# Kernel tuning notes

Measured on AMD Instinct MI355X. Metric: run time of the kernel, lower is better.

## Reference

```python
import jax, jax.numpy as jnp
import numpy as np

NUM_CLASSES = 64
EPSILON = 0.05
BETA1 = 1.0
BETA2 = 1.0
WARM_UP_EPOCH = 10


def _loss(x):
    # log_loss: log(1+exp(-(x-eps))) + log(1+exp(x+eps))
    return jax.nn.softplus(-(x - EPSILON)) + jax.nn.softplus(x + EPSILON)


def _per_class_fac(Y):
    # fac_c = 1 / (N_c * (N_total - N_c)); guarded against degenerate classes
    n = Y.sum(0)
    tot = n.sum()
    ok = (n > 0) & (n < tot)
    return jnp.where(ok, 1.0 / jnp.where(ok, n * (tot - n), 1.0), 0.0)


def _masked_pair_sum(x_cij, Y):
    # x_cij: [C,N,N] pairwise arg; Y: [N,C] one-hot. Sum loss over (pos i, neg j)
    pos = Y.T          # [C,N]
    neg = 1.0 - Y.T    # [C,N]
    return jnp.einsum('cij,ci,cj->c', _loss(x_cij), pos, neg)


def _empirical(preds, Y):
    p = preds.T                              # [C,N]
    d = p[:, :, None] - p[:, None, :]        # [C,N,N] delta_f
    per = _masked_pair_sum(4.0 * (1.0 - d), Y)
    return jnp.sum(_per_class_fac(Y) * per)


def _discrepancy(preds, preds_adv, Y):
    p = preds.T
    pa = preds_adv.T
    d = p[:, :, None] - p[:, None, :]        # delta_f
    da = pa[:, :, None] - pa[:, None, :]     # delta_f_hat
    per = _masked_pair_sum(2.0 * (da - d), Y)
    return jnp.sum(_per_class_fac(Y) * per)


def setup_inputs() -> dict:
    key = jax.random.key(0)
    ks = jax.random.split(key, 5)
    N = 1024
    return {
        'y_s': jax.random.normal(ks[0], (N, NUM_CLASSES), jnp.float32),
        'y_s_adv': jax.random.normal(ks[1], (N, NUM_CLASSES), jnp.float32),
        'labels_s': jax.random.randint(ks[2], (N,), 0, NUM_CLASSES),
        'y_t': jax.random.normal(ks[3], (N, NUM_CLASSES), jnp.float32),
        'y_t_adv': jax.random.normal(ks[4], (N, NUM_CLASSES), jnp.float32),
        'epoch': 10,
    }


def reference(y_s, y_s_adv, labels_s, y_t, y_t_adv, epoch):
    ps = jax.nn.softmax(y_s, axis=-1)
    psa = jax.nn.softmax(y_s_adv, axis=-1)
    Ys = jax.nn.one_hot(labels_s, NUM_CLASSES, dtype=ps.dtype)

    empirical = _empirical(ps, Ys)                      # source empirical AUC error
    src_disc = _discrepancy(ps, psa, Ys)
    transfer = -BETA2 * 0.5 * src_disc

    if epoch >= WARM_UP_EPOCH:  # epoch is a static Python int
        pt = jax.nn.softmax(y_t, axis=-1)
        pta = jax.nn.softmax(y_t_adv, axis=-1)
        # pseudo labels: one-hot of argmax of adversarial-head target probs
        Yt = jax.nn.one_hot(jnp.argmax(pta, axis=-1), NUM_CLASSES, dtype=pt.dtype)
        transfer = transfer + BETA1 * 0.25 * _discrepancy(pt, pta, Yt)

    return (0.25 * empirical, transfer)
```

## Files before the change

kernel.cpp:

```cpp
#include <hip/hip_runtime.h>

#define N 1024
#define C 64
#define CHUNK 256
#define SPLITS (N / CHUNK)

__device__ __forceinline__ float softplus_f(float x) {
    return fmaxf(x, 0.0f) + log1pf(__expf(-fabsf(x)));
}
__device__ __forceinline__ float loss_f(float x) {
    return softplus_f(0.05f - x) + softplus_f(x + 0.05f);
}

__device__ __forceinline__ float softmax64(float x) {
    float m = x;
    #pragma unroll
    for (int off = 32; off; off >>= 1) m = fmaxf(m, __shfl_xor(m, off, 64));
    float e = __expf(x - m);
    float s = e;
    #pragma unroll
    for (int off = 32; off; off >>= 1) s += __shfl_xor(s, off, 64);
    return e / s;
}

__global__ __launch_bounds__(256) void prep_kernel(
    const float* __restrict__ y_s, const float* __restrict__ y_s_adv,
    const float* __restrict__ y_t, const float* __restrict__ y_t_adv,
    float* __restrict__ Ps, float* __restrict__ Qs, float* __restrict__ Qt,
    int* __restrict__ t_labels)
{
    const int lane = threadIdx.x & 63;
    const int row  = blockIdx.x * 4 + (threadIdx.x >> 6);
    if (row >= N) return;
    const int g = row * C + lane;

    float ps  = softmax64(y_s[g]);
    float psa = softmax64(y_s_adv[g]);
    Ps[lane * N + row] = ps;
    Qs[lane * N + row] = psa - ps;

    float xta = y_t_adv[g];
    float pt  = softmax64(y_t[g]);
    float pta = softmax64(xta);
    Qt[lane * N + row] = pta - pt;

    float v = xta; int idx = lane;
    #pragma unroll
    for (int off = 32; off; off >>= 1) {
        float ov = __shfl_xor(v, off, 64);
        int   oi = __shfl_xor(idx, off, 64);
        if (ov > v || (ov == v && oi < idx)) { v = ov; idx = oi; }
    }
    if (lane == 0) t_labels[row] = idx;
}

__global__ __launch_bounds__(256) void pair_kernel(
    const float* __restrict__ Ps, const float* __restrict__ Qs,
    const float* __restrict__ Qt, const int* __restrict__ labels_s,
    const int* __restrict__ t_labels, const int* __restrict__ epoch,
    float* __restrict__ out)
{
    const int b    = blockIdx.x;
    const int s    = b % SPLITS;
    const int c    = (b / SPLITS) % C;
    const int term = b / (SPLITS * C);
    const int tid  = threadIdx.x;

    const int* lab = (term == 2) ? t_labels : labels_s;

    __shared__ int sh_pos[N];
    __shared__ int sh_cnt;
    __shared__ float sh_red[4];
    if (tid == 0) sh_cnt = 0;
    __syncthreads();
    for (int r = tid; r < N; r += 256) {
        if (lab[r] == c) { int k = atomicAdd(&sh_cnt, 1); sh_pos[k] = r; }
    }
    __syncthreads();
    const int n_c = sh_cnt;
    if (n_c == 0 || n_c == N) return;
    const float fac = 1.0f / ((float)n_c * (float)(N - n_c));

    const float* row = ((term == 0) ? Ps : (term == 1) ? Qs : Qt) + c * N;

    float acc = 0.0f;
    const int total = n_c * CHUNK;
    const int j0 = s * CHUNK;
    for (int p = tid; p < total; p += 256) {
        const int j = j0 + (p & (CHUNK - 1));
        if (lab[j] == c) continue;
        const int i = sh_pos[p >> 8];
        const float d = row[i] - row[j];
        const float arg = (term == 0) ? 4.0f * (1.0f - d) : 2.0f * d;
        acc += loss_f(arg);
    }

    #pragma unroll
    for (int off = 32; off; off >>= 1) acc += __shfl_down(acc, off, 64);
    if ((tid & 63) == 0) sh_red[tid >> 6] = acc;
    __syncthreads();
    if (tid == 0) {
        float tot = sh_red[0] + sh_red[1] + sh_red[2] + sh_red[3];
        float scale;
        int slot;
        if (term == 0)      { scale = 0.25f * fac; slot = 0; }
        else if (term == 1) { scale = -0.5f * fac; slot = 1; }
        else { scale = (epoch[0] >= 10) ? 0.25f * fac : 0.0f; slot = 1; }
        atomicAdd(&out[slot], scale * tot);
    }
}

extern "C" void kernel_launch(void* const* d_in, const int* in_sizes, int n_in,
                              void* d_out, int out_size, void* d_ws, size_t ws_size,
                              hipStream_t stream) {
    const float* y_s     = (const float*)d_in[0];
    const float* y_s_adv = (const float*)d_in[1];
    const int*   labels  = (const int*)d_in[2];
    const float* y_t     = (const float*)d_in[3];
    const float* y_t_adv = (const float*)d_in[4];
    const int*   epoch   = (const int*)d_in[5];
    float* out = (float*)d_out;

    float* Ps = (float*)d_ws;
    float* Qs = Ps + C * N;
    float* Qt = Qs + C * N;
    int* t_labels = (int*)(Qt + C * N);

    hipMemsetAsync(d_out, 0, 2 * sizeof(float), stream);

    prep_kernel<<<N / 4, 256, 0, stream>>>(y_s, y_s_adv, y_t, y_t_adv,
                                           Ps, Qs, Qt, t_labels);
    pair_kernel<<<3 * C * SPLITS, 256, 0, stream>>>(Ps, Qs, Qt, labels,
                                                    t_labels, epoch, out);
}
```

Baseline: 96.41 us.

## Stage columns in LDS, merge splits, fuse softplus logs, drop memset

The pair kernel now loads each class column and the labels into shared memory and processes all N negatives per block instead of splitting across four blocks. The two softplus terms are merged into a single fast log of a product of exponentials. The output zeroing moves into the prep kernel, which removes the separate memset launch. The grid shrinks from 768 to 192 blocks, which may underfill the GPU, and the fused log formula can overflow for large arguments.

```diff
diff --git a/kernel.cpp b/kernel.cpp
--- a/kernel.cpp
+++ b/kernel.cpp
@@ -2,14 +2,9 @@
 
 #define N 1024
 #define C 64
-#define CHUNK 256
-#define SPLITS (N / CHUNK)
 
-__device__ __forceinline__ float softplus_f(float x) {
-    return fmaxf(x, 0.0f) + log1pf(__expf(-fabsf(x)));
-}
 __device__ __forceinline__ float loss_f(float x) {
-    return softplus_f(0.05f - x) + softplus_f(x + 0.05f);
+    return __logf((1.0f + __expf(0.05f - x)) * (1.0f + __expf(x + 0.05f)));
 }
 
 __device__ __forceinline__ float softmax64(float x) {
@@ -27,11 +22,12 @@
     const float* __restrict__ y_s, const float* __restrict__ y_s_adv,
     const float* __restrict__ y_t, const float* __restrict__ y_t_adv,
     float* __restrict__ Ps, float* __restrict__ Qs, float* __restrict__ Qt,
-    int* __restrict__ t_labels)
+    int* __restrict__ t_labels, float* __restrict__ out)
 {
+    if (blockIdx.x == 0 && threadIdx.x < 2) out[threadIdx.x] = 0.0f;
+
     const int lane = threadIdx.x & 63;
     const int row  = blockIdx.x * 4 + (threadIdx.x >> 6);
-    if (row >= N) return;
     const int g = row * C + lane;
 
     float ps  = softmax64(y_s[g]);
@@ -60,47 +56,51 @@
     const int* __restrict__ t_labels, const int* __restrict__ epoch,
     float* __restrict__ out)
 {
-    const int b    = blockIdx.x;
-    const int s    = b % SPLITS;
-    const int c    = (b / SPLITS) % C;
-    const int term = b / (SPLITS * C);
+    const int c    = blockIdx.x & 63;
+    const int term = blockIdx.x >> 6;
     const int tid  = threadIdx.x;
 
-    const int* lab = (term == 2) ? t_labels : labels_s;
-
-    __shared__ int sh_pos[N];
-    __shared__ int sh_cnt;
+    __shared__ float sh_col[N];
+    __shared__ int   sh_lab[N];
+    __shared__ int   sh_pos[N];
+    __shared__ int   sh_cnt;
     __shared__ float sh_red[4];
     if (tid == 0) sh_cnt = 0;
-    __syncthreads();
+
+    const int*   lab = (term == 2) ? t_labels : labels_s;
+    const float* col = ((term == 0) ? Ps : (term == 1) ? Qs : Qt) + c * N;
     for (int r = tid; r < N; r += 256) {
-        if (lab[r] == c) { int k = atomicAdd(&sh_cnt, 1); sh_pos[k] = r; }
+        sh_col[r] = col[r];
+        sh_lab[r] = lab[r];
     }
     __syncthreads();
+
+    for (int r = tid; r < N; r += 256)
+        if (sh_lab[r] == c) { int k = atomicAdd(&sh_cnt, 1); sh_pos[k] = r; }
+    __syncthreads();
+
     const int n_c = sh_cnt;
-    if (n_c == 0 || n_c == N) return;
-    const float fac = 1.0f / ((float)n_c * (float)(N - n_c));
-
-    const float* row = ((term == 0) ? Ps : (term == 1) ? Qs : Qt) + c * N;
+    const bool ok = (n_c > 0) && (n_c < N);
 
     float acc = 0.0f;
-    const int total = n_c * CHUNK;
-    const int j0 = s * CHUNK;
-    for (int p = tid; p < total; p += 256) {
-        const int j = j0 + (p & (CHUNK - 1));
-        if (lab[j] == c) continue;
-        const int i = sh_pos[p >> 8];
-        const float d = row[i] - row[j];
-        const float arg = (term == 0) ? 4.0f * (1.0f - d) : 2.0f * d;
-        acc += loss_f(arg);
+    if (ok) {
+        const int total = n_c * N;
+        for (int p = tid; p < total; p += 256) {
+            const int j = p & (N - 1);
+            if (sh_lab[j] == c) continue;
+            const float d = sh_col[sh_pos[p >> 10]] - sh_col[j];
+            const float arg = (term == 0) ? 4.0f * (1.0f - d) : 2.0f * d;
+            acc += loss_f(arg);
+        }
     }
 
     #pragma unroll
     for (int off = 32; off; off >>= 1) acc += __shfl_down(acc, off, 64);
     if ((tid & 63) == 0) sh_red[tid >> 6] = acc;
     __syncthreads();
-    if (tid == 0) {
+    if (tid == 0 && ok) {
         float tot = sh_red[0] + sh_red[1] + sh_red[2] + sh_red[3];
+        float fac = 1.0f / ((float)n_c * (float)(N - n_c));
         float scale;
         int slot;
         if (term == 0)      { scale = 0.25f * fac; slot = 0; }
@@ -126,10 +126,8 @@
     float* Qt = Qs + C * N;
     int* t_labels = (int*)(Qt + C * N);
 
-    hipMemsetAsync(d_out, 0, 2 * sizeof(float), stream);
-
     prep_kernel<<<N / 4, 256, 0, stream>>>(y_s, y_s_adv, y_t, y_t_adv,
-                                           Ps, Qs, Qt, t_labels);
-    pair_kernel<<<3 * C * SPLITS, 256, 0, stream>>>(Ps, Qs, Qt, labels,
-                                                    t_labels, epoch, out);
+                                           Ps, Qs, Qt, t_labels, out);
+    pair_kernel<<<3 * C, 256, 0, stream>>>(Ps, Qs, Qt, labels,
+                                           t_labels, epoch, out);
 }
```

New measurement: 89.85 us. 1.07x faster.
